# Kernel optimization log

Measured on AMD Instinct MI355X. Metric: run time of the kernel, lower is better.

The kernel has to match this reference:

```python
import jax, jax.numpy as jnp
import numpy as np

B, L, D, H, MEM, POL = 32, 256, 768, 12, 384, 3
DK = D // H
ALPHA, BETA, GAMA = 1.0, 0.25, 0.1


def _forward(sequence_output, pooled_output, adj_reshape, src_mask, aspect_mask,
             ln_g, ln_b, wq, bq, wk, bk, wd, bd, weight_m, bias_m,
             wa0, ba0, wa1, ba1, ws0, bs0, ws1, bs1, affine1, affine2, wc, bc):
    b, l, d = sequence_output.shape
    h = weight_m.shape[0]
    dk = d // h

    # custom LayerNorm (torch std is unbiased, ddof=1)
    mu = sequence_output.mean(-1, keepdims=True)
    sd = jnp.std(sequence_output, axis=-1, keepdims=True, ddof=1)
    x = ln_g * (sequence_output - mu) / (sd + 1e-6) + ln_b  # gcn_inputs (dropout = eval identity)

    aspect_outs = x * aspect_mask[:, :, None]

    # multi-head projections  [B,H,L,dk]
    q = (x @ wq + bq).reshape(b, l, h, dk).transpose(0, 2, 1, 3)
    k = (x @ wk + bk).reshape(b, l, h, dk).transpose(0, 2, 1, 3)
    asp = aspect_outs @ wd + bd                       # [B,L,dk]
    asp = jnp.broadcast_to(asp[:, None], (b, h, l, dk))

    # aspect-conditioned scores: tanh(aspect @ W_m @ K^T + b_m)   [B,H,L,L]
    asps = jnp.tanh(jnp.einsum('bhld,hde,bhme->bhlm', asp, weight_m, k) + bias_m[0])
    avg = asps.sum(axis=-2) / l                       # [B,H,L]

    # fusion overwrite: for each aspect index idx, row idx and col idx <- avg.
    # Sequential loop semantics (ascending idx, row-then-col) collapse to:
    #   both aspect (i,j): value = avg[min(i,j)];  row-only: avg[j];  col-only: avg[i]
    is_asp = aspect_mask > 0                          # [B,L]
    rowm = is_asp[:, None, :, None]
    colm = is_asp[:, None, None, :]
    avg_i = avg[..., :, None]                         # [B,H,L,1]
    avg_j = avg[..., None, :]                         # [B,H,1,L]
    ge = (jnp.arange(l)[:, None] >= jnp.arange(l)[None, :])  # i>=j -> min=j
    both_val = jnp.where(ge, avg_j, avg_i)
    aspect_scores = jnp.where(rowm & colm, both_val,
                      jnp.where(rowm, avg_j,
                        jnp.where(colm, avg_i, asps)))

    # standard scaled-dot attention
    scores = jnp.einsum('bhld,bhmd->bhlm', q, k) / jnp.sqrt(jnp.float32(dk))
    scores = jnp.where(src_mask[:, None, None, :] == 0, -1e9, scores)
    s_attn = jax.nn.softmax(scores, axis=-1)          # dropout = eval identity

    aspect_score_avg = aspect_scores.mean(axis=1)     # [B,L,L]
    adj_s = s_attn.mean(axis=1)                       # [B,L,L]

    eye = jnp.eye(l, dtype=adj_s.dtype)
    adj_s = adj_s * (1.0 - eye) + eye                 # zero diag then add identity
    adj_s = src_mask[:, :, None] * adj_s

    adj_r = jnp.exp(ALPHA * adj_reshape)
    dist_mask = aspect_score_avg > BETA
    adj_r = jnp.where(dist_mask, 1.0, adj_r)
    adj_ag = adj_r * aspect_score_avg

    log_p = jax.nn.log_softmax(adj_ag, axis=-1)
    log_q = jax.nn.log_softmax(adj_s, axis=-1)
    q_t = jnp.exp(log_q)
    kl = jnp.sum(q_t * (log_q - log_p))
    kl_loss = jnp.exp(-1.0 * kl * GAMA)

    denom_s = adj_s.sum(axis=2, keepdims=True) + 1.0
    denom_ag = adj_ag.sum(axis=2, keepdims=True) + 1.0

    out_ag, out_s = x, x
    was = [(wa0, ba0), (wa1, ba1)]
    wss = [(ws0, bs0), (ws1, bs1)]
    for li in range(2):
        g_ag = jax.nn.relu(((adj_ag @ out_ag) @ was[li][0] + was[li][1]) / denom_ag)
        g_s = jax.nn.relu(((adj_s @ out_s) @ wss[li][0] + wss[li][1]) / denom_s)
        A1 = jax.nn.softmax(jnp.einsum('bld,de,bme->blm', g_ag, affine1, g_s), axis=-1)
        A2 = jax.nn.softmax(jnp.einsum('bld,de,bme->blm', g_s, affine2, g_ag), axis=-1)
        out_ag = A1 @ g_s
        out_s = A2 @ g_ag   # gcn_drop = eval identity

    asp_wn = aspect_mask.sum(axis=1, keepdims=True)   # [B,1]
    m = aspect_mask[:, :, None]
    outputs1 = (out_ag * m).sum(axis=1) / asp_wn      # [B,MEM]
    outputs2 = (out_s * m).sum(axis=1) / asp_wn

    final = jnp.concatenate([outputs1, outputs2, pooled_output], axis=-1) @ wc + bc
    return final, kl_loss


def setup_inputs() -> dict:
    key = jax.random.key(0)
    ks = jax.random.split(key, 16)
    s = 0.02
    pos = jnp.arange(L)
    start = 5 + (jnp.arange(B) % 16)
    aspect_mask = ((pos[None, :] >= start[:, None]) & (pos[None, :] < start[:, None] + 3)).astype(jnp.float32)
    f32 = jnp.float32
    return {
        'sequence_output': jax.random.normal(ks[0], (B, L, D), f32),
        'pooled_output': jax.random.normal(ks[1], (B, D), f32),
        'adj_reshape': jax.random.uniform(ks[2], (B, L, L), f32),
        'src_mask': jnp.ones((B, L), f32),
        'aspect_mask': aspect_mask,
        'ln_g': jnp.ones((D,), f32), 'ln_b': jnp.zeros((D,), f32),
        'wq': jax.random.normal(ks[3], (D, D), f32) * s, 'bq': jnp.zeros((D,), f32),
        'wk': jax.random.normal(ks[4], (D, D), f32) * s, 'bk': jnp.zeros((D,), f32),
        'wd': jax.random.normal(ks[5], (D, DK), f32) * s, 'bd': jnp.zeros((DK,), f32),
        'weight_m': jax.random.normal(ks[6], (H, DK, DK), f32) * s,
        'bias_m': jnp.zeros((1,), f32),
        'wa0': jax.random.normal(ks[7], (D, MEM), f32) * s, 'ba0': jnp.zeros((MEM,), f32),
        'wa1': jax.random.normal(ks[8], (MEM, MEM), f32) * s, 'ba1': jnp.zeros((MEM,), f32),
        'ws0': jax.random.normal(ks[9], (D, MEM), f32) * s, 'bs0': jnp.zeros((MEM,), f32),
        'ws1': jax.random.normal(ks[10], (MEM, MEM), f32) * s, 'bs1': jnp.zeros((MEM,), f32),
        'affine1': jax.random.normal(ks[11], (MEM, MEM), f32) * s,
        'affine2': jax.random.normal(ks[12], (MEM, MEM), f32) * s,
        'wc': jax.random.normal(ks[13], (2 * D, POL), f32) * s, 'bc': jnp.zeros((POL,), f32),
    }


def reference(sequence_output, pooled_output, adj_reshape, src_mask, aspect_mask,
              ln_g, ln_b, wq, bq, wk, bk, wd, bd, weight_m, bias_m,
              wa0, ba0, wa1, ba1, ws0, bs0, ws1, bs1, affine1, affine2, wc, bc):
    return _forward(sequence_output, pooled_output, adj_reshape, src_mask, aspect_mask,
                    ln_g, ln_b, wq, bq, wk, bk, wd, bd, weight_m, bias_m,
                    wa0, ba0, wa1, ba1, ws0, bs0, ws1, bs1, affine1, affine2, wc, bc)
```

## Files before the change

### kernel.cpp

```cpp
#include <hip/hip_runtime.h>

#define B_ 32
#define L_ 256
#define D_ 768
#define H_ 12
#define DK_ 64
#define MEM_ 384

typedef __attribute__((ext_vector_type(8))) short bfrag8;
typedef __attribute__((ext_vector_type(8))) unsigned short us8;
typedef __attribute__((ext_vector_type(4))) float f32x4;

__device__ inline unsigned short f2bf(float f) {
  unsigned u = __float_as_uint(f);
  return (unsigned short)((u + 0x7fffu + ((u >> 16) & 1u)) >> 16);
}
__device__ inline float bf2f(unsigned short u) {
  return __uint_as_float(((unsigned)u) << 16);
}
__device__ inline float tanh_fast(float x) {
  x = fminf(fmaxf(x, -30.f), 30.f);
  float e = __expf(2.f * x);
  return (e - 1.f) * __builtin_amdgcn_rcpf(e + 1.f);
}
__device__ inline void gload_lds16(const unsigned short* g, unsigned short* l) {
  __builtin_amdgcn_global_load_lds(
      (__attribute__((address_space(1))) void*)(g),
      (__attribute__((address_space(3))) void*)(l), 16, 0, 0);
}

__device__ inline float waveRedSum(float v) {
#pragma unroll
  for (int o = 32; o; o >>= 1) v += __shfl_xor(v, o, 64);
  return v;
}
__device__ inline float waveRedMax(float v) {
#pragma unroll
  for (int o = 32; o; o >>= 1) v = fmaxf(v, __shfl_xor(v, o, 64));
  return v;
}
__device__ inline float blkRedSum(float v, float* red) {
  v = waveRedSum(v);
  int w = threadIdx.x >> 6;
  __syncthreads();
  if ((threadIdx.x & 63) == 0) red[w] = v;
  __syncthreads();
  return red[0] + red[1] + red[2] + red[3];
}
__device__ inline float blkRedMax(float v, float* red) {
  v = waveRedMax(v);
  int w = threadIdx.x >> 6;
  __syncthreads();
  if ((threadIdx.x & 63) == 0) red[w] = v;
  __syncthreads();
  return fmaxf(fmaxf(red[0], red[1]), fmaxf(red[2], red[3]));
}

__global__ __launch_bounds__(256) void prep_kernel(
    const float* __restrict__ seq, const float* __restrict__ lng,
    const float* __restrict__ lnb, float* __restrict__ xout,
    unsigned short* __restrict__ xbf,
    const float* __restrict__ wq, unsigned short* __restrict__ wqT,
    const float* __restrict__ wk, unsigned short* __restrict__ wkT,
    const float* __restrict__ wa0, unsigned short* __restrict__ wa0T,
    const float* __restrict__ ws0, unsigned short* __restrict__ ws0T,
    const float* __restrict__ wa1, unsigned short* __restrict__ wa1T,
    const float* __restrict__ ws1, unsigned short* __restrict__ ws1T,
    const float* __restrict__ aff1, unsigned short* __restrict__ aff1T,
    const float* __restrict__ aff2, unsigned short* __restrict__ aff2T,
    const float* __restrict__ wd, unsigned short* __restrict__ wdT,
    const float* __restrict__ wm, unsigned short* __restrict__ wmT) {
  int bid = blockIdx.x;
  if (bid >= 600) {
    long row = bid - 600;
    const float* p = seq + row * D_;
    float v[3];
#pragma unroll
    for (int i = 0; i < 3; ++i) v[i] = p[threadIdx.x + i * 256];
    __shared__ float red[4];
    float s = v[0] + v[1] + v[2];
    s = blkRedSum(s, red);
    float mu = s * (1.f / D_);
    float ss = 0.f;
#pragma unroll
    for (int i = 0; i < 3; ++i) { float d = v[i] - mu; ss += d * d; }
    ss = blkRedSum(ss, red);
    float sd = sqrtf(ss * (1.f / (D_ - 1)));
    float inv = 1.f / (sd + 1e-6f);
#pragma unroll
    for (int i = 0; i < 3; ++i) {
      int c = threadIdx.x + i * 256;
      float o = lng[c] * (v[i] - mu) * inv + lnb[c];
      xout[row * D_ + c] = o;
      xbf[row * D_ + c] = f2bf(o);
    }
    return;
  }
  const float* src; unsigned short* dst; int Rr, Cc, tIdx;
  if (bid < 144)      { src = wq;   dst = wqT;   Rr = 768; Cc = 768; tIdx = bid; }
  else if (bid < 288) { src = wk;   dst = wkT;   Rr = 768; Cc = 768; tIdx = bid - 144; }
  else if (bid < 360) { src = wa0;  dst = wa0T;  Rr = 768; Cc = 384; tIdx = bid - 288; }
  else if (bid < 432) { src = ws0;  dst = ws0T;  Rr = 768; Cc = 384; tIdx = bid - 360; }
  else if (bid < 468) { src = wa1;  dst = wa1T;  Rr = 384; Cc = 384; tIdx = bid - 432; }
  else if (bid < 504) { src = ws1;  dst = ws1T;  Rr = 384; Cc = 384; tIdx = bid - 468; }
  else if (bid < 540) { src = aff1; dst = aff1T; Rr = 384; Cc = 384; tIdx = bid - 504; }
  else if (bid < 576) { src = aff2; dst = aff2T; Rr = 384; Cc = 384; tIdx = bid - 540; }
  else if (bid < 588) { src = wd;   dst = wdT;   Rr = 768; Cc = 64;  tIdx = bid - 576; }
  else { int h = bid - 588; src = wm + h * 4096; dst = wmT + h * 4096; Rr = 64; Cc = 64; tIdx = 0; }
  __shared__ float tile[64][65];
  int nx = Cc >> 6;
  int c0 = (tIdx % nx) * 64, r0 = (tIdx / nx) * 64;
  int tx = threadIdx.x & 63, ty = threadIdx.x >> 6;
#pragma unroll
  for (int i = 0; i < 16; ++i)
    tile[ty + i * 4][tx] = src[(long)(r0 + ty + i * 4) * Cc + c0 + tx];
  __syncthreads();
#pragma unroll
  for (int i = 0; i < 16; ++i)
    dst[(long)(c0 + ty + i * 4) * Rr + r0 + tx] = f2bf(tile[tx][ty + i * 4]);
}

template <int MR>
__global__ __launch_bounds__(256) void gemm_bb(
    const unsigned short* __restrict__ A, const unsigned short* __restrict__ Bt,
    float* __restrict__ C, unsigned short* __restrict__ Cbf,
    unsigned short* __restrict__ CT,
    int M, int N, int K, long sA, long sB, long sC, long sCT,
    const float* __restrict__ bias, const float* __restrict__ rowDiv, int relu,
    const unsigned short* __restrict__ A2, const unsigned short* __restrict__ Bt2,
    float* __restrict__ C2, unsigned short* __restrict__ Cbf2,
    unsigned short* __restrict__ CT2,
    const float* __restrict__ bias2, const float* __restrict__ rowDiv2, int zsplit) {
  constexpr int MFRAG = MR / 32;
  constexpr int RW = MR / 2;
  constexpr int ASH = MR * 32;
  constexpr int BUFS = ASH + 4096;
  constexpr int TSH = 64 * (MR + 8);
  constexpr int SMN = (2 * BUFS > TSH) ? 2 * BUFS : TSH;
  __shared__ alignas(16) unsigned short smem[SMN];
  const int tid = threadIdx.x;
  const int bn = blockIdx.x, bm = blockIdx.y;
  int bz = blockIdx.z;
  const unsigned short* Ap = A; const unsigned short* Btp = Bt;
  float* Cp = C; unsigned short* Cbp = Cbf; unsigned short* CTp = CT;
  const float* biasp = bias; const float* rowDivp = rowDiv;
  if (zsplit > 0 && bz >= zsplit) {
    bz -= zsplit;
    Ap = A2; Btp = Bt2; Cp = C2; Cbp = Cbf2; CTp = CT2; biasp = bias2; rowDivp = rowDiv2;
  }
  Ap += (long)bz * sA; Btp += (long)bz * sB;
  if (Cp) Cp += (long)bz * sC;
  if (Cbp) Cbp += (long)bz * sC;
  if (CTp) CTp += (long)bz * sCT;

  f32x4 acc[MFRAG][4] = {};
  const int l = tid & 63, w = tid >> 6;
  const int wr = w >> 1, wc = w & 1;
  const int lr = l & 15, sg = l >> 4;

  const int rc = l >> 2;
  const int sslot = (l & 3) ^ ((rc >> 1) & 3);
  const unsigned short* gA0 = Ap + (long)(bm * MR + w * 16 + rc) * K + sslot * 8;
  const unsigned short* gA1 = (MR == 128)
      ? Ap + (long)(bm * MR + (w + 4) * 16 + rc) * K + sslot * 8 : nullptr;
  const unsigned short* gB0 = Btp + (long)(bn * 128 + w * 16 + rc) * K + sslot * 8;
  const unsigned short* gB1 = Btp + (long)(bn * 128 + (w + 4) * 16 + rc) * K + sslot * 8;
  const int stA0 = w * 512, stA1 = (w + 4) * 512;
  const int stB0 = ASH + w * 512, stB1 = ASH + (w + 4) * 512;

  const int swz = (sg ^ ((lr >> 1) & 3)) * 8;
  int aoff[MFRAG], boff[4];
#pragma unroll
  for (int m = 0; m < MFRAG; ++m) aoff[m] = (wr * RW + m * 16 + lr) * 32 + swz;
#pragma unroll
  for (int n = 0; n < 4; ++n) boff[n] = ASH + (wc * 64 + n * 16 + lr) * 32 + swz;

  const int nt = K >> 5;
  gload_lds16(gA0, smem + stA0);
  if (MR == 128) gload_lds16(gA1, smem + stA1);
  gload_lds16(gB0, smem + stB0);
  gload_lds16(gB1, smem + stB1);
  __syncthreads();

  for (int t = 0; t < nt; ++t) {
    const int cur = (t & 1) * BUFS;
    if (t + 1 < nt) {
      const int nxt = ((t + 1) & 1) * BUFS;
      const int k1 = (t + 1) << 5;
      gload_lds16(gA0 + k1, smem + nxt + stA0);
      if (MR == 128) gload_lds16(gA1 + k1, smem + nxt + stA1);
      gload_lds16(gB0 + k1, smem + nxt + stB0);
      gload_lds16(gB1 + k1, smem + nxt + stB1);
    }
    bfrag8 af[MFRAG], bf[4];
#pragma unroll
    for (int m = 0; m < MFRAG; ++m) af[m] = *(const bfrag8*)(smem + cur + aoff[m]);
#pragma unroll
    for (int n = 0; n < 4; ++n) bf[n] = *(const bfrag8*)(smem + cur + boff[n]);
#pragma unroll
    for (int m = 0; m < MFRAG; ++m)
#pragma unroll
      for (int n = 0; n < 4; ++n)
        acc[m][n] = __builtin_amdgcn_mfma_f32_16x16x32_bf16(af[m], bf[n], acc[m][n], 0, 0, 0);
    __syncthreads();
  }

  if (Cp || Cbp) {
#pragma unroll
    for (int m = 0; m < MFRAG; ++m) {
#pragma unroll
      for (int r = 0; r < 4; ++r) {
        int row = bm * MR + wr * RW + m * 16 + (l >> 4) * 4 + r;
        float rd = rowDivp ? 1.f / rowDivp[(long)bz * M + row] : 1.f;
#pragma unroll
        for (int n = 0; n < 4; ++n) {
          int col = bn * 128 + wc * 64 + n * 16 + lr;
          float v = acc[m][n][r];
          if (biasp) v += biasp[col];
          v *= rd;
          if (relu) v = fmaxf(v, 0.f);
          if (Cp) Cp[(long)row * N + col] = v;
          if (Cbp) Cbp[(long)row * N + col] = f2bf(v);
        }
      }
    }
  }
  if (CT) {
    auto Ts = (unsigned short(*)[MR + 8])smem;
#pragma unroll
    for (int ch = 0; ch < 2; ++ch) {
      __syncthreads();
      if (wc == ch) {
#pragma unroll
        for (int m = 0; m < MFRAG; ++m) {
#pragma unroll
          for (int r = 0; r < 4; ++r) {
            int rowl = wr * RW + m * 16 + (l >> 4) * 4 + r;
            float rd = rowDivp ? 1.f / rowDivp[(long)bz * M + bm * MR + rowl] : 1.f;
#pragma unroll
            for (int n = 0; n < 4; ++n) {
              int col = bn * 128 + wc * 64 + n * 16 + lr;
              float v = acc[m][n][r];
              if (biasp) v += biasp[col];
              v *= rd;
              if (relu) v = fmaxf(v, 0.f);
              Ts[n * 16 + lr][rowl] = f2bf(v);
            }
          }
        }
      }
      __syncthreads();
      int trow = tid >> 2, tc = (tid & 3) * (MR / 4);
      int colg = bn * 128 + ch * 64 + trow;
      int rowg = bm * MR + tc;
      unsigned short* dp = CTp + (long)(rowg >> 8) * sCT + (long)colg * 256 + (rowg & 255);
#pragma unroll
      for (int j = 0; j < MR / 32; ++j)
        *(us8*)(dp + j * 8) = *(const us8*)&Ts[trow][tc + j * 8];
    }
  }
}

__global__ __launch_bounds__(256) void attn_asp(
    const unsigned short* __restrict__ qbf, const unsigned short* __restrict__ kbf,
    const float* __restrict__ srcm,
    float* __restrict__ part0, float* __restrict__ part1,
    const unsigned short* __restrict__ xbf, const unsigned short* __restrict__ wdT,
    const float* __restrict__ amask, const float* __restrict__ bd,
    unsigned short* __restrict__ aspbf) {
  int t = threadIdx.x;
  int w = t >> 6, l = t & 63;
  int lr = l & 15, kg = (l >> 4) * 8;
  if (blockIdx.x >= 1024) {
    int l0 = (blockIdx.x - 1024) << 4;
    const unsigned short* ap = xbf + (long)(l0 + lr) * D_ + kg;
    const unsigned short* bp = wdT + (long)(w * 16 + lr) * D_ + kg;
    f32x4 acc = {};
#pragma unroll
    for (int k0 = 0; k0 < D_; k0 += 32) {
      bfrag8 af = *(const bfrag8*)(ap + k0);
      bfrag8 bf = *(const bfrag8*)(bp + k0);
      acc = __builtin_amdgcn_mfma_f32_16x16x32_bf16(af, bf, acc, 0, 0, 0);
    }
    int col = w * 16 + lr;
#pragma unroll
    for (int r = 0; r < 4; ++r) {
      int row = l0 + (l >> 4) * 4 + r;
      float v = acc[r] * amask[row] + bd[col];
      aspbf[(long)row * DK_ + col] = f2bf(v);
    }
    return;
  }
  int d = blockIdx.x;
  int b = (d & 7) + 8 * ((d >> 3) & 3);
  int rest = d >> 5;
  int l0 = (rest & 15) << 4;
  int half = rest >> 4;
  int rbase = (l >> 4) * 4;
  __shared__ float red[3][2][16][8];
  float acc[4][4] = {};
  float cmv[4];
#pragma unroll
  for (int ct = 0; ct < 4; ++ct) cmv[ct] = srcm[b * L_ + w * 64 + ct * 16 + lr];

#pragma unroll 1
  for (int ph = 0; ph < 3; ++ph) {
    int hp = half * 3 + ph;
    const unsigned short* ap = qbf + ((long)b * L_ + l0 + lr) * D_ + hp * 128 + kg;
    bfrag8 a00 = *(const bfrag8*)ap;
    bfrag8 a01 = *(const bfrag8*)(ap + 32);
    bfrag8 a10 = *(const bfrag8*)(ap + 64);
    bfrag8 a11 = *(const bfrag8*)(ap + 96);
    bfrag8 kv[4][4];
#pragma unroll
    for (int ct = 0; ct < 4; ++ct) {
      const unsigned short* bp =
          kbf + ((long)b * L_ + w * 64 + ct * 16 + lr) * D_ + hp * 128 + kg;
      kv[ct][0] = *(const bfrag8*)bp;
      kv[ct][1] = *(const bfrag8*)(bp + 32);
      kv[ct][2] = *(const bfrag8*)(bp + 64);
      kv[ct][3] = *(const bfrag8*)(bp + 96);
    }
    float sv0[4][4], sv1[4][4];
#pragma unroll
    for (int ct = 0; ct < 4; ++ct) {
      f32x4 c0 = {}, c1 = {};
      c0 = __builtin_amdgcn_mfma_f32_16x16x32_bf16(a00, kv[ct][0], c0, 0, 0, 0);
      c0 = __builtin_amdgcn_mfma_f32_16x16x32_bf16(a01, kv[ct][1], c0, 0, 0, 0);
      c1 = __builtin_amdgcn_mfma_f32_16x16x32_bf16(a10, kv[ct][2], c1, 0, 0, 0);
      c1 = __builtin_amdgcn_mfma_f32_16x16x32_bf16(a11, kv[ct][3], c1, 0, 0, 0);
      bool msk = (cmv[ct] == 0.f);
#pragma unroll
      for (int r = 0; r < 4; ++r) {
        sv0[ct][r] = msk ? -1e9f : c0[r] * 0.125f;
        sv1[ct][r] = msk ? -1e9f : c1[r] * 0.125f;
      }
    }
    float mx0a[4], mx1a[4];
#pragma unroll
    for (int r = 0; r < 4; ++r) {
      float m0 = fmaxf(fmaxf(sv0[0][r], sv0[1][r]), fmaxf(sv0[2][r], sv0[3][r]));
      float m1 = fmaxf(fmaxf(sv1[0][r], sv1[1][r]), fmaxf(sv1[2][r], sv1[3][r]));
#pragma unroll
      for (int o = 1; o < 16; o <<= 1) {
        m0 = fmaxf(m0, __shfl_xor(m0, o, 64));
        m1 = fmaxf(m1, __shfl_xor(m1, o, 64));
      }
      mx0a[r] = m0; mx1a[r] = m1;
      float s0 = 0.f, s1 = 0.f;
#pragma unroll
      for (int ct = 0; ct < 4; ++ct) {
        float e0 = __expf(sv0[ct][r] - m0);
        float e1 = __expf(sv1[ct][r] - m1);
        sv0[ct][r] = e0; sv1[ct][r] = e1;
        s0 += e0; s1 += e1;
      }
#pragma unroll
      for (int o = 1; o < 16; o <<= 1) {
        s0 += __shfl_xor(s0, o, 64);
        s1 += __shfl_xor(s1, o, 64);
      }
      if (lr == 0) {
        red[ph][0][rbase + r][w] = m0;
        red[ph][0][rbase + r][4 + w] = s0;
        red[ph][1][rbase + r][w] = m1;
        red[ph][1][rbase + r][4 + w] = s1;
      }
    }
    __syncthreads();
#pragma unroll
    for (int r = 0; r < 4; ++r) {
      f32x4 m4 = *(const f32x4*)&red[ph][0][rbase + r][0];
      f32x4 s4 = *(const f32x4*)&red[ph][0][rbase + r][4];
      float mt = fmaxf(fmaxf(m4[0], m4[1]), fmaxf(m4[2], m4[3]));
      float tot = s4[0] * __expf(m4[0] - mt) + s4[1] * __expf(m4[1] - mt) +
                  s4[2] * __expf(m4[2] - mt) + s4[3] * __expf(m4[3] - mt);
      float sc0 = __expf(mx0a[r] - mt) * __builtin_amdgcn_rcpf(tot);
      f32x4 n4 = *(const f32x4*)&red[ph][1][rbase + r][0];
      f32x4 t4 = *(const f32x4*)&red[ph][1][rbase + r][4];
      float nt = fmaxf(fmaxf(n4[0], n4[1]), fmaxf(n4[2], n4[3]));
      float tt = t4[0] * __expf(n4[0] - nt) + t4[1] * __expf(n4[1] - nt) +
                 t4[2] * __expf(n4[2] - nt) + t4[3] * __expf(n4[3] - nt);
      float sc1 = __expf(mx1a[r] - nt) * __builtin_amdgcn_rcpf(tt);
#pragma unroll
      for (int ct = 0; ct < 4; ++ct)
        acc[ct][r] += sv0[ct][r] * sc0 + sv1[ct][r] * sc1;
    }
  }

  float* pp = half ? part1 : part0;
#pragma unroll
  for (int r = 0; r < 4; ++r) {
    int row = l0 + rbase + r;
#pragma unroll
    for (int ct = 0; ct < 4; ++ct) {
      int col = w * 64 + ct * 16 + lr;
      pp[((long)b * L_ + row) * L_ + col] = acc[ct][r];
    }
  }
}

__global__ __launch_bounds__(256) void asp_wm_v2(const unsigned short* __restrict__ aspbf,
                                                 const unsigned short* __restrict__ wmT,
                                                 unsigned short* __restrict__ tmpA) {
  int bh = blockIdx.x;
  int b = bh / H_, h = bh % H_;
  int t = threadIdx.x;
  int w = t >> 6, l = t & 63;
  int lr = l & 15, kg = (l >> 4) * 8;
  const unsigned short* wp = wmT + h * 4096;
  f32x4 acc[4][4] = {};
#pragma unroll
  for (int ks = 0; ks < 2; ++ks) {
    int k0 = ks * 32;
    bfrag8 af[4], bf[4];
#pragma unroll
    for (int m = 0; m < 4; ++m)
      af[m] = *(const bfrag8*)(aspbf + (long)(b * L_ + w * 64 + m * 16 + lr) * DK_ + k0 + kg);
#pragma unroll
    for (int n = 0; n < 4; ++n)
      bf[n] = *(const bfrag8*)(wp + (n * 16 + lr) * 64 + k0 + kg);
#pragma unroll
    for (int m = 0; m < 4; ++m)
#pragma unroll
      for (int n = 0; n < 4; ++n)
        acc[m][n] = __builtin_amdgcn_mfma_f32_16x16x32_bf16(af[m], bf[n], acc[m][n], 0, 0, 0);
  }
#pragma unroll
  for (int m = 0; m < 4; ++m)
#pragma unroll
    for (int n = 0; n < 4; ++n)
#pragma unroll
      for (int r = 0; r < 4; ++r) {
        int row = w * 64 + m * 16 + (l >> 4) * 4 + r;
        int col = n * 16 + lr;
        tmpA[(((long)b * H_ + h) * L_ + row) * DK_ + col] = f2bf(acc[m][n][r]);
      }
}

__global__ __launch_bounds__(256) void gemm_sfmx(
    const unsigned short* __restrict__ u1, const unsigned short* __restrict__ g1,
    unsigned short* __restrict__ P1,
    const unsigned short* __restrict__ u2, const unsigned short* __restrict__ g2,
    unsigned short* __restrict__ P2) {
  constexpr int ASH = 64 * 32;
  constexpr int BUFS = ASH + 8192;
  __shared__ alignas(16) unsigned short smem[2 * BUFS];
  __shared__ float redm[2][64];
  __shared__ float reds[2][64];
  int bm = blockIdx.x;
  int bz = blockIdx.y;
  const unsigned short* Ap; const unsigned short* Bp; unsigned short* Pp;
  if (bz < 32) {
    Ap = u1 + (long)bz * L_ * MEM_; Bp = g1 + (long)bz * L_ * MEM_;
    Pp = P1 + (long)bz * L_ * L_;
  } else {
    int z = bz - 32;
    Ap = u2 + (long)z * L_ * MEM_; Bp = g2 + (long)z * L_ * MEM_;
    Pp = P2 + (long)z * L_ * L_;
  }
  const int t = threadIdx.x;
  const int l = t & 63, w = t >> 6;
  const int wr = w >> 1, wc = w & 1;
  const int lr = l & 15, sg = l >> 4;
  f32x4 acc[2][8] = {};

  const int rc = l >> 2;
  const int sslot = (l & 3) ^ ((rc >> 1) & 3);
  const unsigned short* gA = Ap + (long)(bm * 64 + w * 16 + rc) * MEM_ + sslot * 8;
  const unsigned short* gB[4];
#pragma unroll
  for (int j = 0; j < 4; ++j)
    gB[j] = Bp + (long)(w * 64 + j * 16 + rc) * MEM_ + sslot * 8;
  const int stA = w * 512;
  int stB[4];
#pragma unroll
  for (int j = 0; j < 4; ++j) stB[j] = ASH + (w * 4 + j) * 512;

  const int swz = (sg ^ ((lr >> 1) & 3)) * 8;
  int aoff[2], boff[8];
#pragma unroll
  for (int m = 0; m < 2; ++m) aoff[m] = (wr * 32 + m * 16 + lr) * 32 + swz;
#pragma unroll
  for (int n = 0; n < 8; ++n) boff[n] = ASH + (wc * 128 + n * 16 + lr) * 32 + swz;

  gload_lds16(gA, smem + stA);
#pragma unroll
  for (int j = 0; j < 4; ++j) gload_lds16(gB[j], smem + stB[j]);
  __syncthreads();

  constexpr int NT = MEM_ / 32;
  for (int tt = 0; tt < NT; ++tt) {
    const int cur = (tt & 1) * BUFS;
    if (tt + 1 < NT) {
      const int nxt = ((tt + 1) & 1) * BUFS;
      const int k1 = (tt + 1) << 5;
      gload_lds16(gA + k1, smem + nxt + stA);
#pragma unroll
      for (int j = 0; j < 4; ++j) gload_lds16(gB[j] + k1, smem + nxt + stB[j]);
    }
    bfrag8 af[2], bf[8];
#pragma unroll
    for (int m = 0; m < 2; ++m) af[m] = *(const bfrag8*)(smem + cur + aoff[m]);
#pragma unroll
    for (int n = 0; n < 8; ++n) bf[n] = *(const bfrag8*)(smem + cur + boff[n]);
#pragma unroll
    for (int m = 0; m < 2; ++m)
#pragma unroll
      for (int n = 0; n < 8; ++n)
        acc[m][n] = __builtin_amdgcn_mfma_f32_16x16x32_bf16(af[m], bf[n], acc[m][n], 0, 0, 0);
    __syncthreads();
  }

#pragma unroll
  for (int m = 0; m < 2; ++m) {
#pragma unroll
    for (int r = 0; r < 4; ++r) {
      int lrow = wr * 32 + m * 16 + (l >> 4) * 4 + r;
      float mx = -1e30f;
#pragma unroll
      for (int n = 0; n < 8; ++n) mx = fmaxf(mx, acc[m][n][r]);
#pragma unroll
      for (int o = 1; o < 16; o <<= 1) mx = fmaxf(mx, __shfl_xor(mx, o, 64));
      if (lr == 0) redm[wc][lrow] = mx;
    }
  }
  __syncthreads();
#pragma unroll
  for (int m = 0; m < 2; ++m) {
#pragma unroll
    for (int r = 0; r < 4; ++r) {
      int lrow = wr * 32 + m * 16 + (l >> 4) * 4 + r;
      float mx = fmaxf(redm[0][lrow], redm[1][lrow]);
      float s = 0.f;
#pragma unroll
      for (int n = 0; n < 8; ++n) {
        float e = __expf(acc[m][n][r] - mx);
        acc[m][n][r] = e;
        s += e;
      }
#pragma unroll
      for (int o = 1; o < 16; o <<= 1) s += __shfl_xor(s, o, 64);
      if (lr == 0) reds[wc][lrow] = s;
    }
  }
  __syncthreads();
#pragma unroll
  for (int m = 0; m < 2; ++m) {
#pragma unroll
    for (int r = 0; r < 4; ++r) {
      int lrow = wr * 32 + m * 16 + (l >> 4) * 4 + r;
      float inv = 1.f / (reds[0][lrow] + reds[1][lrow]);
      int row = bm * 64 + lrow;
#pragma unroll
      for (int n = 0; n < 8; ++n) {
        int col = wc * 128 + n * 16 + lr;
        Pp[(long)row * L_ + col] = f2bf(acc[m][n][r] * inv);
      }
    }
  }
}

__global__ __launch_bounds__(256) void asps_mean_v2(
    const unsigned short* __restrict__ tmpA,
    const unsigned short* __restrict__ kbf,
    const float* __restrict__ bias_m,
    float* __restrict__ asps_mean) {
  int blk = blockIdx.x;
  int b = blk >> 4, l0 = (blk & 15) << 4;
  int t = threadIdx.x;
  int w = t >> 6, l = t & 63;
  int lr = l & 15, kg = (l >> 4) * 8;
  float bm = bias_m[0];
  float accg[4][4] = {};
  for (int h = 0; h < H_; ++h) {
    const unsigned short* ap = tmpA + (((long)b * H_ + h) * L_ + l0 + lr) * 64 + kg;
    bfrag8 af0 = *(const bfrag8*)ap;
    bfrag8 af1 = *(const bfrag8*)(ap + 32);
#pragma unroll
    for (int ct = 0; ct < 4; ++ct) {
      const unsigned short* bp =
          kbf + ((long)b * L_ + w * 64 + ct * 16 + lr) * D_ + h * 64 + kg;
      bfrag8 bf0 = *(const bfrag8*)bp;
      bfrag8 bf1 = *(const bfrag8*)(bp + 32);
      f32x4 accl = {};
      accl = __builtin_amdgcn_mfma_f32_16x16x32_bf16(af0, bf0, accl, 0, 0, 0);
      accl = __builtin_amdgcn_mfma_f32_16x16x32_bf16(af1, bf1, accl, 0, 0, 0);
#pragma unroll
      for (int r = 0; r < 4; ++r) accg[ct][r] += tanh_fast(accl[r] + bm);
    }
  }
#pragma unroll
  for (int ct = 0; ct < 4; ++ct) {
    int col = w * 64 + ct * 16 + lr;
#pragma unroll
    for (int r = 0; r < 4; ++r) {
      int row = l0 + (l >> 4) * 4 + r;
      asps_mean[((long)b * L_ + row) * L_ + col] = accg[ct][r] * (1.f / H_);
    }
  }
}

__global__ __launch_bounds__(1024) void avgh_kernel(const float* __restrict__ asps_mean,
                                                    float* __restrict__ avgH) {
  int b = blockIdx.x;
  int m = threadIdx.x & 255, q = threadIdx.x >> 8;
  __shared__ float part[4][256];
  float s = 0.f;
  for (int l = q * 64; l < q * 64 + 64; ++l)
    s += asps_mean[((long)b * L_ + l) * L_ + m];
  part[q][m] = s;
  __syncthreads();
  if (q == 0)
    avgH[b * L_ + m] = (part[0][m] + part[1][m] + part[2][m] + part[3][m]) * (1.f / L_);
}

__global__ __launch_bounds__(256) void adjag_kl(const float* __restrict__ part0,
                                                const float* __restrict__ part1,
                                                const float* __restrict__ srcm,
                                                const float* __restrict__ asps_mean,
                                                const float* __restrict__ avgH,
                                                const float* __restrict__ amask,
                                                const float* __restrict__ adjr,
                                                unsigned short* __restrict__ adjsbf,
                                                unsigned short* __restrict__ adjagbf,
                                                float* __restrict__ klpart,
                                                float* __restrict__ den_s,
                                                float* __restrict__ den_ag) {
  long row = blockIdx.x;
  int m = threadIdx.x;
  int l = (int)(row & 255);
  int b = (int)(row >> 8);
  long idx = row * L_ + m;
  float s = (part0[idx] + part1[idx]) * (1.f / H_);
  if (m == l) s = 1.f;
  s *= srcm[b * L_ + l];
  adjsbf[idx] = f2bf(s);
  bool rowa = amask[b * L_ + l] > 0.f;
  bool cola = amask[b * L_ + m] > 0.f;
  float asa;
  if (rowa && cola) asa = (l >= m) ? avgH[b * L_ + m] : avgH[b * L_ + l];
  else if (rowa)    asa = avgH[b * L_ + m];
  else if (cola)    asa = avgH[b * L_ + l];
  else              asa = asps_mean[idx];
  float r = (asa > 0.25f) ? 1.f : expf(adjr[idx]);
  float a = r * asa;
  adjagbf[idx] = f2bf(a);

  __shared__ float red[4];
  float sum_s = blkRedSum(s, red);
  float sum_a = blkRedSum(a, red);
  float mx_s = blkRedMax(s, red);
  float mx_a = blkRedMax(a, red);
  float es = expf(s - mx_s), ea = expf(a - mx_a);
  float ses = blkRedSum(es, red);
  float sea = blkRedSum(ea, red);
  float logq = (s - mx_s) - logf(ses);
  float logp = (a - mx_a) - logf(sea);
  float term = (es / ses) * (logq - logp);
  float kp = blkRedSum(term, red);
  if (m == 0) {
    klpart[row] = kp;
    den_s[row] = sum_s + 1.f;
    den_ag[row] = sum_a + 1.f;
  }
}

__global__ __launch_bounds__(256) void final_kernel(const unsigned short* __restrict__ o_ag,
                                                    const unsigned short* __restrict__ o_s,
                                                    const float* __restrict__ pooled,
                                                    const float* __restrict__ amask,
                                                    const float* __restrict__ wc,
                                                    const float* __restrict__ bc,
                                                    const float* __restrict__ klpart,
                                                    float* __restrict__ dout) {
  int b = blockIdx.x, t = threadIdx.x;
  __shared__ float red[4];
  if (b == B_) {
    float s = 0.f;
    for (int i = t; i < B_ * L_; i += 256) s += klpart[i];
    s = blkRedSum(s, red);
    if (t == 0) dout[96] = expf(-s * 0.1f);
    return;
  }
  __shared__ float cS[1536];
  __shared__ float maskS[256];
  maskS[t] = amask[b * L_ + t];
  float wn = blkRedSum(maskS[t], red);
  for (int e = t; e < MEM_; e += 256) {
    float s1 = 0.f, s2 = 0.f;
    for (int l = 0; l < L_; ++l) {
      float mk = maskS[l];
      if (mk != 0.f) {
        s1 += mk * bf2f(o_ag[((long)b * L_ + l) * MEM_ + e]);
        s2 += mk * bf2f(o_s[((long)b * L_ + l) * MEM_ + e]);
      }
    }
    cS[e] = s1 / wn;
    cS[MEM_ + e] = s2 / wn;
  }
  for (int j = t; j < D_; j += 256) cS[2 * MEM_ + j] = pooled[b * D_ + j];
  __syncthreads();
  float p0 = 0.f, p1 = 0.f, p2 = 0.f;
  for (int j = t; j < 1536; j += 256) {
    float v = cS[j];
    p0 += v * wc[j * 3 + 0];
    p1 += v * wc[j * 3 + 1];
    p2 += v * wc[j * 3 + 2];
  }
  p0 = blkRedSum(p0, red);
  p1 = blkRedSum(p1, red);
  p2 = blkRedSum(p2, red);
  if (t == 0) {
    dout[b * 3 + 0] = p0 + bc[0];
    dout[b * 3 + 1] = p1 + bc[1];
    dout[b * 3 + 2] = p2 + bc[2];
  }
}

extern "C" void kernel_launch(void* const* d_in, const int* in_sizes, int n_in,
                              void* d_out, int out_size, void* d_ws, size_t ws_size,
                              hipStream_t stream) {
  const float* seq    = (const float*)d_in[0];
  const float* pooled = (const float*)d_in[1];
  const float* adjr   = (const float*)d_in[2];
  const float* srcm   = (const float*)d_in[3];
  const float* amask  = (const float*)d_in[4];
  const float* ln_g   = (const float*)d_in[5];
  const float* ln_b   = (const float*)d_in[6];
  const float* wq     = (const float*)d_in[7];
  const float* bq     = (const float*)d_in[8];
  const float* wk     = (const float*)d_in[9];
  const float* bk     = (const float*)d_in[10];
  const float* wd     = (const float*)d_in[11];
  const float* bd     = (const float*)d_in[12];
  const float* wm     = (const float*)d_in[13];
  const float* bm     = (const float*)d_in[14];
  const float* wa0    = (const float*)d_in[15];
  const float* ba0    = (const float*)d_in[16];
  const float* wa1    = (const float*)d_in[17];
  const float* ba1    = (const float*)d_in[18];
  const float* ws0    = (const float*)d_in[19];
  const float* bs0    = (const float*)d_in[20];
  const float* ws1    = (const float*)d_in[21];
  const float* bs1    = (const float*)d_in[22];
  const float* aff1   = (const float*)d_in[23];
  const float* aff2   = (const float*)d_in[24];
  const float* wc     = (const float*)d_in[25];
  const float* bc     = (const float*)d_in[26];

  float* ws = (float*)d_ws;
  float* S0 = ws;
  float* S1 = S0 + 6291456;
  float* S2 = S1 + 3145728;
  float* S3 = S2 + 3145728;
  float* S4 = S3 + 3145728;
  float* S5 = S4 + 524288;
  float* part0  = S5 + 2097152;
  float* part1  = part0 + 2097152;
  unsigned short* adjsbf  = (unsigned short*)(part1 + 2097152);
  unsigned short* adjagbf = adjsbf + 2097152;
  unsigned short* wT      = adjagbf + 2097152;
  unsigned short* wqT   = wT;
  unsigned short* wkT   = wT + 589824;
  unsigned short* wa0T  = wT + 1179648;
  unsigned short* ws0T  = wT + 1474560;
  unsigned short* wa1T  = wT + 1769472;
  unsigned short* ws1T  = wT + 1916928;
  unsigned short* aff1T = wT + 2064384;
  unsigned short* aff2T = wT + 2211840;
  float* tail   = (float*)(wT + 2359296);
  float* avgH   = tail;
  float* den_s  = avgH + 8192;
  float* den_ag = den_s + 8192;
  float* klp    = den_ag + 8192;

  float* x = S0;
  unsigned short* o_agbf = (unsigned short*)S0;
  unsigned short* o_sbf  = o_agbf + 3145728;
  unsigned short* gTag   = o_agbf + 6291456;
  unsigned short* gTs    = o_agbf + 9437184;
  unsigned short* xbf    = (unsigned short*)S1;
  unsigned short* qbf    = (unsigned short*)S2;
  unsigned short* tmpA   = (unsigned short*)S2;
  unsigned short* g_agbf = (unsigned short*)S2;
  unsigned short* g_sbf  = g_agbf + 3145728;
  unsigned short* kbf    = (unsigned short*)S3;
  unsigned short* tTag   = (unsigned short*)S3;
  unsigned short* tTs    = tTag + 3145728;
  unsigned short* u1bf   = (unsigned short*)S3;
  unsigned short* u2bf   = u1bf + 3145728;
  unsigned short* aspbf  = (unsigned short*)S4;
  unsigned short* wdT    = aspbf + 524288;
  unsigned short* wmT    = wdT + 49152;
  float* asps = S5;
  unsigned short* P1bf = (unsigned short*)S5;
  unsigned short* P2bf = P1bf + 2097152;
  float* dout = (float*)d_out;

  const long sAdjSh = (long)L_ * L_;
  const long sMemSh = (long)L_ * MEM_;

  prep_kernel<<<600 + B_ * L_, 256, 0, stream>>>(
      seq, ln_g, ln_b, x, xbf, wq, wqT, wk, wkT, wa0, wa0T, ws0, ws0T,
      wa1, wa1T, ws1, ws1T, aff1, aff1T, aff2, aff2T, wd, wdT, wm, wmT);
  gemm_bb<128><<<dim3(6, 64, 2), 256, 0, stream>>>(
      xbf, wqT, nullptr, qbf, nullptr, 8192, 768, 768, 0, 0, 0, 0, bq, nullptr, 0,
      xbf, wkT, nullptr, kbf, nullptr, bk, nullptr, 1);
  attn_asp<<<1536, 256, 0, stream>>>(qbf, kbf, srcm, part0, part1,
                                     xbf, wdT, amask, bd, aspbf);
  asp_wm_v2<<<B_ * H_, 256, 0, stream>>>(aspbf, wmT, tmpA);
  asps_mean_v2<<<B_ * 16, 256, 0, stream>>>(tmpA, kbf, bm, asps);
  avgh_kernel<<<B_, 1024, 0, stream>>>(asps, avgH);
  adjag_kl<<<B_ * L_, 256, 0, stream>>>(part0, part1, srcm, asps, avgH, amask, adjr,
                                        adjsbf, adjagbf, klp, den_s, den_ag);

  for (int li = 0; li < 2; ++li) {
    int Kd = li ? MEM_ : D_;
    const unsigned short* inag = li ? o_agbf : xbf;
    const unsigned short* ins  = li ? o_sbf : xbf;
    const unsigned short* wAT = li ? wa1T : wa0T;
    const float* bA = li ? ba1 : ba0;
    const unsigned short* wST = li ? ws1T : ws0T;
    const float* bS = li ? bs1 : bs0;
    gemm_bb<64><<<dim3(3, 128, 2), 256, 0, stream>>>(
        inag, wAT, nullptr, nullptr, tTag, 8192, MEM_, Kd, 0, 0, 0, sMemSh,
        nullptr, nullptr, 0,
        ins, wST, nullptr, nullptr, tTs, nullptr, nullptr, 1);
    gemm_bb<64><<<dim3(3, 4, 64), 256, 0, stream>>>(
        adjagbf, tTag, nullptr, g_agbf, gTag, L_, MEM_, L_, sAdjSh, sMemSh, sMemSh,
        sMemSh, bA, den_ag, 1,
        adjsbf, tTs, nullptr, g_sbf, gTs, bS, den_s, 32);
    gemm_bb<64><<<dim3(3, 128, 2), 256, 0, stream>>>(
        g_agbf, aff1T, nullptr, u1bf, nullptr, 8192, MEM_, MEM_, 0, 0, 0, 0,
        nullptr, nullptr, 0,
        g_sbf, aff2T, nullptr, u2bf, nullptr, nullptr, nullptr, 1);
    gemm_sfmx<<<dim3(4, 64), 256, 0, stream>>>(u1bf, g_sbf, P1bf, u2bf, g_agbf, P2bf);
    gemm_bb<64><<<dim3(3, 4, 64), 256, 0, stream>>>(
        P1bf, gTs, nullptr, o_agbf, nullptr, L_, MEM_, L_, sAdjSh, sMemSh, sMemSh, 0,
        nullptr, nullptr, 0,
        P2bf, gTag, nullptr, o_sbf, nullptr, nullptr, nullptr, 32);
  }

  final_kernel<<<B_ + 1, 256, 0, stream>>>(o_agbf, o_sbf, pooled, amask, wc, bc,
                                           klp, dout);
}
```

Measured before the change: 395.2 us.

## Restructure attention so each wave owns full rows and writes bf16 adj_s directly

The self-attention scores kernel is reorganised so each wave computes full 256-column rows for 16 query rows across all 12 heads, using transposed MFMA (K as A operand) so softmax reductions need only two cross-lane shuffles and no shared-memory combine or block sync. The head-average, diagonal override and source-mask scaling are fused into its epilogue, which writes bf16 adj_s directly instead of two fp32 partial buffers. This removes the fp32 partial traffic and its re-read in adjag_kl, which now loads the bf16 values. In exchange there are fewer blocks (128 attention blocks), high register pressure from a 16x4 accumulator plus a 16x4 score array, and adj_s values used in later sums are bf16-rounded.

```diff
diff --git a/kernel.cpp b/kernel.cpp
--- a/kernel.cpp
+++ b/kernel.cpp
@@ -9,6 +9,7 @@
 
 typedef __attribute__((ext_vector_type(8))) short bfrag8;
 typedef __attribute__((ext_vector_type(8))) unsigned short us8;
+typedef __attribute__((ext_vector_type(4))) unsigned short us4;
 typedef __attribute__((ext_vector_type(4))) float f32x4;
 
 __device__ inline unsigned short f2bf(float f) {
@@ -264,15 +265,15 @@
 __global__ __launch_bounds__(256) void attn_asp(
     const unsigned short* __restrict__ qbf, const unsigned short* __restrict__ kbf,
     const float* __restrict__ srcm,
-    float* __restrict__ part0, float* __restrict__ part1,
+    unsigned short* __restrict__ adjsbf,
     const unsigned short* __restrict__ xbf, const unsigned short* __restrict__ wdT,
     const float* __restrict__ amask, const float* __restrict__ bd,
     unsigned short* __restrict__ aspbf) {
   int t = threadIdx.x;
   int w = t >> 6, l = t & 63;
-  int lr = l & 15, kg = (l >> 4) * 8;
-  if (blockIdx.x >= 1024) {
-    int l0 = (blockIdx.x - 1024) << 4;
+  if (blockIdx.x >= 128) {
+    int lr = l & 15, kg = (l >> 4) * 8;
+    int l0 = (blockIdx.x - 128) << 4;
     const unsigned short* ap = xbf + (long)(l0 + lr) * D_ + kg;
     const unsigned short* bp = wdT + (long)(w * 16 + lr) * D_ + kg;
     f32x4 acc = {};
@@ -291,112 +292,81 @@
     }
     return;
   }
-  int d = blockIdx.x;
-  int b = (d & 7) + 8 * ((d >> 3) & 3);
-  int rest = d >> 5;
-  int l0 = (rest & 15) << 4;
-  int half = rest >> 4;
-  int rbase = (l >> 4) * 4;
-  __shared__ float red[3][2][16][8];
-  float acc[4][4] = {};
-  float cmv[4];
-#pragma unroll
-  for (int ct = 0; ct < 4; ++ct) cmv[ct] = srcm[b * L_ + w * 64 + ct * 16 + lr];
-
+  int blk = blockIdx.x;
+  int b = blk & 31;
+  int slice = (blk >> 5) * 4 + w;
+  int l0 = slice << 4;
+  int qr = l & 15, hi = l >> 4;
+  int row = l0 + qr;
+  long qbase = ((long)b * L_ + row) * D_;
+  float rm = srcm[b * L_ + row];
+
+  unsigned long long mbits = 0ull;
+#pragma unroll
+  for (int ct = 0; ct < 16; ++ct) {
+    float4 c4 = *(const float4*)&srcm[b * L_ + ct * 16 + hi * 4];
+    mbits |= (unsigned long long)(c4.x != 0.f) << (ct * 4 + 0);
+    mbits |= (unsigned long long)(c4.y != 0.f) << (ct * 4 + 1);
+    mbits |= (unsigned long long)(c4.z != 0.f) << (ct * 4 + 2);
+    mbits |= (unsigned long long)(c4.w != 0.f) << (ct * 4 + 3);
+  }
+
+  float acc[16][4] = {};
 #pragma unroll 1
-  for (int ph = 0; ph < 3; ++ph) {
-    int hp = half * 3 + ph;
-    const unsigned short* ap = qbf + ((long)b * L_ + l0 + lr) * D_ + hp * 128 + kg;
-    bfrag8 a00 = *(const bfrag8*)ap;
-    bfrag8 a01 = *(const bfrag8*)(ap + 32);
-    bfrag8 a10 = *(const bfrag8*)(ap + 64);
-    bfrag8 a11 = *(const bfrag8*)(ap + 96);
-    bfrag8 kv[4][4];
-#pragma unroll
-    for (int ct = 0; ct < 4; ++ct) {
-      const unsigned short* bp =
-          kbf + ((long)b * L_ + w * 64 + ct * 16 + lr) * D_ + hp * 128 + kg;
-      kv[ct][0] = *(const bfrag8*)bp;
-      kv[ct][1] = *(const bfrag8*)(bp + 32);
-      kv[ct][2] = *(const bfrag8*)(bp + 64);
-      kv[ct][3] = *(const bfrag8*)(bp + 96);
-    }
-    float sv0[4][4], sv1[4][4];
-#pragma unroll
-    for (int ct = 0; ct < 4; ++ct) {
-      f32x4 c0 = {}, c1 = {};
-      c0 = __builtin_amdgcn_mfma_f32_16x16x32_bf16(a00, kv[ct][0], c0, 0, 0, 0);
-      c0 = __builtin_amdgcn_mfma_f32_16x16x32_bf16(a01, kv[ct][1], c0, 0, 0, 0);
-      c1 = __builtin_amdgcn_mfma_f32_16x16x32_bf16(a10, kv[ct][2], c1, 0, 0, 0);
-      c1 = __builtin_amdgcn_mfma_f32_16x16x32_bf16(a11, kv[ct][3], c1, 0, 0, 0);
-      bool msk = (cmv[ct] == 0.f);
+  for (int h = 0; h < H_; ++h) {
+    bfrag8 qf0 = *(const bfrag8*)(qbf + qbase + h * 64 + hi * 8);
+    bfrag8 qf1 = *(const bfrag8*)(qbf + qbase + h * 64 + 32 + hi * 8);
+    float sv[16][4];
+    float mx = -1e30f;
+#pragma unroll
+    for (int ct = 0; ct < 16; ++ct) {
+      const unsigned short* kp =
+          kbf + ((long)b * L_ + ct * 16 + qr) * D_ + h * 64 + hi * 8;
+      bfrag8 kf0 = *(const bfrag8*)kp;
+      bfrag8 kf1 = *(const bfrag8*)(kp + 32);
+      f32x4 c = {};
+      c = __builtin_amdgcn_mfma_f32_16x16x32_bf16(kf0, qf0, c, 0, 0, 0);
+      c = __builtin_amdgcn_mfma_f32_16x16x32_bf16(kf1, qf1, c, 0, 0, 0);
 #pragma unroll
       for (int r = 0; r < 4; ++r) {
-        sv0[ct][r] = msk ? -1e9f : c0[r] * 0.125f;
-        sv1[ct][r] = msk ? -1e9f : c1[r] * 0.125f;
+        float v = ((mbits >> (ct * 4 + r)) & 1ull) ? c[r] * 0.125f : -1e9f;
+        sv[ct][r] = v;
+        mx = fmaxf(mx, v);
       }
     }
-    float mx0a[4], mx1a[4];
+    mx = fmaxf(mx, __shfl_xor(mx, 16, 64));
+    mx = fmaxf(mx, __shfl_xor(mx, 32, 64));
+    float sum = 0.f;
+#pragma unroll
+    for (int ct = 0; ct < 16; ++ct)
+#pragma unroll
+      for (int r = 0; r < 4; ++r) {
+        float e = __expf(sv[ct][r] - mx);
+        sv[ct][r] = e;
+        sum += e;
+      }
+    sum += __shfl_xor(sum, 16, 64);
+    sum += __shfl_xor(sum, 32, 64);
+    float inv = __builtin_amdgcn_rcpf(sum);
+#pragma unroll
+    for (int ct = 0; ct < 16; ++ct)
+#pragma unroll
+      for (int r = 0; r < 4; ++r) acc[ct][r] += sv[ct][r] * inv;
+  }
+
+  long obase = ((long)b * L_ + row) * L_;
+#pragma unroll
+  for (int ct = 0; ct < 16; ++ct) {
+    us4 pk;
 #pragma unroll
     for (int r = 0; r < 4; ++r) {
-      float m0 = fmaxf(fmaxf(sv0[0][r], sv0[1][r]), fmaxf(sv0[2][r], sv0[3][r]));
-      float m1 = fmaxf(fmaxf(sv1[0][r], sv1[1][r]), fmaxf(sv1[2][r], sv1[3][r]));
-#pragma unroll
-      for (int o = 1; o < 16; o <<= 1) {
-        m0 = fmaxf(m0, __shfl_xor(m0, o, 64));
-        m1 = fmaxf(m1, __shfl_xor(m1, o, 64));
-      }
-      mx0a[r] = m0; mx1a[r] = m1;
-      float s0 = 0.f, s1 = 0.f;
-#pragma unroll
-      for (int ct = 0; ct < 4; ++ct) {
-        float e0 = __expf(sv0[ct][r] - m0);
-        float e1 = __expf(sv1[ct][r] - m1);
-        sv0[ct][r] = e0; sv1[ct][r] = e1;
-        s0 += e0; s1 += e1;
-      }
-#pragma unroll
-      for (int o = 1; o < 16; o <<= 1) {
-        s0 += __shfl_xor(s0, o, 64);
-        s1 += __shfl_xor(s1, o, 64);
-      }
-      if (lr == 0) {
-        red[ph][0][rbase + r][w] = m0;
-        red[ph][0][rbase + r][4 + w] = s0;
-        red[ph][1][rbase + r][w] = m1;
-        red[ph][1][rbase + r][4 + w] = s1;
-      }
-    }
-    __syncthreads();
-#pragma unroll
-    for (int r = 0; r < 4; ++r) {
-      f32x4 m4 = *(const f32x4*)&red[ph][0][rbase + r][0];
-      f32x4 s4 = *(const f32x4*)&red[ph][0][rbase + r][4];
-      float mt = fmaxf(fmaxf(m4[0], m4[1]), fmaxf(m4[2], m4[3]));
-      float tot = s4[0] * __expf(m4[0] - mt) + s4[1] * __expf(m4[1] - mt) +
-                  s4[2] * __expf(m4[2] - mt) + s4[3] * __expf(m4[3] - mt);
-      float sc0 = __expf(mx0a[r] - mt) * __builtin_amdgcn_rcpf(tot);
-      f32x4 n4 = *(const f32x4*)&red[ph][1][rbase + r][0];
-      f32x4 t4 = *(const f32x4*)&red[ph][1][rbase + r][4];
-      float nt = fmaxf(fmaxf(n4[0], n4[1]), fmaxf(n4[2], n4[3]));
-      float tt = t4[0] * __expf(n4[0] - nt) + t4[1] * __expf(n4[1] - nt) +
-                 t4[2] * __expf(n4[2] - nt) + t4[3] * __expf(n4[3] - nt);
-      float sc1 = __expf(mx1a[r] - nt) * __builtin_amdgcn_rcpf(tt);
-#pragma unroll
-      for (int ct = 0; ct < 4; ++ct)
-        acc[ct][r] += sv0[ct][r] * sc0 + sv1[ct][r] * sc1;
-    }
-  }
-
-  float* pp = half ? part1 : part0;
-#pragma unroll
-  for (int r = 0; r < 4; ++r) {
-    int row = l0 + rbase + r;
-#pragma unroll
-    for (int ct = 0; ct < 4; ++ct) {
-      int col = w * 64 + ct * 16 + lr;
-      pp[((long)b * L_ + row) * L_ + col] = acc[ct][r];
-    }
+      int col = ct * 16 + hi * 4 + r;
+      float v = acc[ct][r] * (1.f / H_);
+      if (col == row) v = 1.f;
+      v *= rm;
+      pk[r] = f2bf(v);
+    }
+    *(us4*)(adjsbf + obase + ct * 16 + hi * 4) = pk;
   }
 }
 
@@ -615,14 +585,11 @@
     avgH[b * L_ + m] = (part[0][m] + part[1][m] + part[2][m] + part[3][m]) * (1.f / L_);
 }
 
-__global__ __launch_bounds__(256) void adjag_kl(const float* __restrict__ part0,
-                                                const float* __restrict__ part1,
-                                                const float* __restrict__ srcm,
+__global__ __launch_bounds__(256) void adjag_kl(const unsigned short* __restrict__ adjsbf,
                                                 const float* __restrict__ asps_mean,
                                                 const float* __restrict__ avgH,
                                                 const float* __restrict__ amask,
                                                 const float* __restrict__ adjr,
-                                                unsigned short* __restrict__ adjsbf,
                                                 unsigned short* __restrict__ adjagbf,
                                                 float* __restrict__ klpart,
                                                 float* __restrict__ den_s,
@@ -632,10 +599,7 @@
   int l = (int)(row & 255);
   int b = (int)(row >> 8);
   long idx = row * L_ + m;
-  float s = (part0[idx] + part1[idx]) * (1.f / H_);
-  if (m == l) s = 1.f;
-  s *= srcm[b * L_ + l];
-  adjsbf[idx] = f2bf(s);
+  float s = bf2f(adjsbf[idx]);
   bool rowa = amask[b * L_ + l] > 0.f;
   bool cola = amask[b * L_ + m] > 0.f;
   float asa;
@@ -807,13 +771,13 @@
   gemm_bb<128><<<dim3(6, 64, 2), 256, 0, stream>>>(
       xbf, wqT, nullptr, qbf, nullptr, 8192, 768, 768, 0, 0, 0, 0, bq, nullptr, 0,
       xbf, wkT, nullptr, kbf, nullptr, bk, nullptr, 1);
-  attn_asp<<<1536, 256, 0, stream>>>(qbf, kbf, srcm, part0, part1,
-                                     xbf, wdT, amask, bd, aspbf);
+  attn_asp<<<640, 256, 0, stream>>>(qbf, kbf, srcm, adjsbf,
+                                    xbf, wdT, amask, bd, aspbf);
   asp_wm_v2<<<B_ * H_, 256, 0, stream>>>(aspbf, wmT, tmpA);
   asps_mean_v2<<<B_ * 16, 256, 0, stream>>>(tmpA, kbf, bm, asps);
   avgh_kernel<<<B_, 1024, 0, stream>>>(asps, avgH);
-  adjag_kl<<<B_ * L_, 256, 0, stream>>>(part0, part1, srcm, asps, avgH, amask, adjr,
-                                        adjsbf, adjagbf, klp, den_s, den_ag);
+  adjag_kl<<<B_ * L_, 256, 0, stream>>>(adjsbf, asps, avgH, amask, adjr,
+                                        adjagbf, klp, den_s, den_ag);
 
   for (int li = 0; li < 2; ++li) {
     int Kd = li ? MEM_ : D_;
```

Result: slower. 443.3 us (+12.2%).
